# Optimization experiments

Hardware: AMD Instinct MI355X
Metric: run time of the kernel (lower is better)

## Reference

```python
import jax, jax.numpy as jnp
import numpy as np

N, E = 8192, 256
NUM_CLASSES = 4
MARGIN = 0.5
EPS = 1e-8  # torch F.cosine_similarity eps


def setup_inputs() -> dict:
    key = jax.random.key(0)
    k1, k2 = jax.random.split(key)
    inp = jax.random.normal(k1, (N, E), dtype=jnp.float32)
    target = jax.random.randint(k2, (N,), 0, NUM_CLASSES, dtype=jnp.int64)
    return {"input": inp, "target": target}


def reference(input, target):
    n, e = input.shape
    # cosine similarity via normalized matmul (QK^T style) instead of O(N^2 E) broadcast
    norm = jnp.maximum(jnp.linalg.norm(input, axis=1), EPS)
    xn = input / norm[:, None]                      # [N, E]
    cossim = xn @ xn.T                              # [N, N]

    triu = jnp.triu(jnp.ones((n, n), dtype=bool), k=1)  # strict upper triangle

    # initial same_class_mask from binary target; overwritten in the loop below
    binary = target > 0
    same_class_mask = binary[:, None] == binary[None, :]

    same_class_loss = jnp.zeros((), dtype=input.dtype)
    for i in range(NUM_CLASSES):
        is_i = target == i
        cnt = jnp.sum(is_i).astype(input.dtype)
        mask_i = is_i[:, None] == is_i[None, :]     # matches (target==i) vs (target==i) outer equality
        # torch computes target_a == target_b with both being (target==i):
        # equal when both True OR both False
        term = jnp.sum((1.0 - cossim) * (mask_i & triu).astype(input.dtype))
        same_class_loss = same_class_loss + jnp.where(
            cnt > 0, term / jnp.maximum(cnt, 1.0), 0.0
        )
        # torch's loop leaves same_class_mask equal to the last class with counts > 0
        same_class_mask = jnp.where(cnt > 0, mask_i, same_class_mask)

    diff = jax.nn.relu(cossim * (~same_class_mask).astype(input.dtype) - MARGIN)
    diff_class_loss = jnp.sum(diff * triu.astype(input.dtype))

    return (same_class_loss + diff_class_loss) / n
```

## Files before the change

### kernel.cpp

```cpp
#include <hip/hip_runtime.h>

#define NROWS 8192
#define CNT_OFF   0
#define CTR_OFF   16
#define P2_OFF    64
#define H_OFF     4096
#define IDXNL_OFF 8192
#define IDXL_OFF  24576
#define CS_OFF    65536
#define XN_OFF    1048576

typedef __bf16 bf16x8 __attribute__((ext_vector_type(8)));
typedef float  f32x4  __attribute__((ext_vector_type(4)));

__device__ __forceinline__ unsigned short f2bf(float f) {
  unsigned int u = __float_as_uint(f);
  u += 0x7fffu + ((u >> 16) & 1u);
  return (unsigned short)(u >> 16);
}

__device__ __forceinline__ void gl_lds16(const void* g, void* l) {
  __builtin_amdgcn_global_load_lds(
      (const __attribute__((address_space(1))) unsigned int*)g,
      (__attribute__((address_space(3))) unsigned int*)l, 16, 0, 0);
}

__global__ __launch_bounds__(1024) void k_normcs(const float* __restrict__ x,
                                                 const int* __restrict__ tgt,
                                                 unsigned short* __restrict__ xn,
                                                 int* __restrict__ h,
                                                 float* __restrict__ cs) {
  __shared__ float lx[64][256];
  __shared__ int lt[64];
  __shared__ int lh[4];
  const int tid = threadIdx.x, w = tid >> 6, lane = tid & 63;
  const int b = blockIdx.x;
  if (tid < 4) lh[tid] = 0;
  if (tid < 64) lt[tid] = tgt[b * 64 + tid];
#pragma unroll
  for (int i = 0; i < 4; ++i) {
    int r = w * 4 + i;
    int row = b * 64 + r;
    float4 v = reinterpret_cast<const float4*>(x)[row * 64 + lane];
    float ss = v.x * v.x + v.y * v.y + v.z * v.z + v.w * v.w;
#pragma unroll
    for (int off = 32; off; off >>= 1) ss += __shfl_xor(ss, off);
    float iv = 1.0f / fmaxf(sqrtf(ss), 1e-8f);
    float4 nv = make_float4(v.x * iv, v.y * iv, v.z * iv, v.w * iv);
    ushort4 o;
    o.x = f2bf(nv.x); o.y = f2bf(nv.y); o.z = f2bf(nv.z); o.w = f2bf(nv.w);
    reinterpret_cast<ushort4*>(xn)[row * 64 + lane] = o;
    *reinterpret_cast<float4*>(&lx[r][lane * 4]) = nv;
  }
  __syncthreads();
  if (tid < 64) atomicAdd(&lh[lt[tid]], 1);
  {
    const int c = tid >> 8, col = tid & 255;
    float m = 0.0f;
#pragma unroll 8
    for (int r = 0; r < 64; ++r)
      m += (lt[r] == c) ? lx[r][col] : 0.0f;
    cs[b * 1024 + tid] = m;
  }
  __syncthreads();
  if (tid < 4) h[b * 4 + tid] = lh[tid];
}

__global__ __launch_bounds__(256) void k_part(const int* __restrict__ tgt,
                                              const int* __restrict__ h,
                                              int* __restrict__ cnt,
                                              int* __restrict__ ctr,
                                              unsigned short* __restrict__ idxNL,
                                              unsigned short* __restrict__ idxL) {
  __shared__ int lcnt[4], lnb, lwc[4];
  const int tid = threadIdx.x, w = tid >> 6, lane = tid & 63;
  if (tid < 4) lcnt[tid] = 0;
  if (tid == 0) lnb = 0;
  __syncthreads();
  if (tid < 128) {
    int4 hv = ((const int4*)h)[tid];
    atomicAdd(&lcnt[0], hv.x); atomicAdd(&lcnt[1], hv.y);
    atomicAdd(&lcnt[2], hv.z); atomicAdd(&lcnt[3], hv.w);
  }
  __syncthreads();
  int L = 0;
#pragma unroll
  for (int i = 0; i < 4; ++i) if (lcnt[i] > 0) L = i;
  if (tid < 4 * blockIdx.x) atomicAdd(&lnb, h[tid * 4 + L]);
  int r = blockIdx.x * 256 + tid;
  bool isL = (tgt[r] == L);
  unsigned long long mk = __ballot(isL);
  int nl = __popcll(mk);
  if (lane == 0) lwc[w] = nl;
  __syncthreads();
  int baseL = lnb, baseN = blockIdx.x * 256 - lnb;
  for (int w2 = 0; w2 < w; ++w2) { baseL += lwc[w2]; baseN += 64 - lwc[w2]; }
  int pos = __popcll(mk & ((1ull << lane) - 1ull));
  if (isL) idxL[baseL + pos] = (unsigned short)r;
  else     idxNL[baseN + (lane - pos)] = (unsigned short)r;
  if (blockIdx.x == 0 && tid < 4) cnt[tid] = lcnt[tid];
  if (blockIdx.x == 0 && tid == 0) { ctr[1] = lcnt[L]; ctr[0] = NROWS - lcnt[L]; }
}

__global__ __launch_bounds__(256, 2) void k_main(const char* __restrict__ xnb,
                                                 const unsigned short* __restrict__ idxNL,
                                                 const unsigned short* __restrict__ idxL,
                                                 const int* __restrict__ ctr,
                                                 float* __restrict__ partial) {
  __shared__ char lds[2][32768];
  __shared__ float wred[4];

  const int tid = threadIdx.x;
  const int w = tid >> 6, l = tid & 63;
  const int M = ctr[0], NL = ctr[1];
  const int ni = (M + 127) >> 7, nj = (NL + 127) >> 7;
  const int ntiles = ni * nj;

  const int rloc = (l >> 3);
  const unsigned pe = ((unsigned)((l & 7) ^ rloc)) << 4;
  const int wr = (w >> 1) * 64, wc = (w & 1) * 64;
  const int l15 = l & 15;
  const unsigned q16 = ((unsigned)(l >> 4)) << 4;
  const unsigned key = ((unsigned)(l & 7)) << 4;
  const int rowj = (l >> 4) * 4;

  float bsum = 0.0f;
  for (int t = blockIdx.x; t < ntiles; t += gridDim.x) {
    int bi = t / nj, bj = t - bi * nj;
    int rm = min(128, M - bi * 128);
    int rn = min(128, NL - bj * 128);
    bool full = (rm == 128) && (rn == 128);

    unsigned aoff[4], boff[4];
#pragma unroll
    for (int j = 0; j < 4; ++j) {
      int row = (j * 4 + w) * 8 + rloc;
      int ga = idxNL[bi * 128 + min(row, rm - 1)];
      int gb = idxL [bj * 128 + min(row, rn - 1)];
      aoff[j] = (unsigned)ga * 512u + pe;
      boff[j] = (unsigned)gb * 512u + pe;
    }

    auto stage = [&](int buf, int ch) {
      unsigned cbo = (unsigned)(ch << 7);
#pragma unroll
      for (int j = 0; j < 4; ++j)
        gl_lds16(xnb + (size_t)(aoff[j] + cbo), &lds[buf][(j * 4 + w) * 1024]);
#pragma unroll
      for (int j = 0; j < 4; ++j)
        gl_lds16(xnb + (size_t)(boff[j] + cbo), &lds[buf][16384 + (j * 4 + w) * 1024]);
    };

    f32x4 acc[4][4];
#pragma unroll
    for (int m = 0; m < 4; ++m)
#pragma unroll
      for (int n = 0; n < 4; ++n)
        acc[m][n] = (f32x4){0.f, 0.f, 0.f, 0.f};

    auto compute = [&](int buf) {
      const char* bA = lds[buf];
      const char* bB = lds[buf] + 16384;
#pragma unroll
      for (int ks = 0; ks < 2; ++ks) {
        const unsigned q = (unsigned)(ks * 64) + q16;
        bf16x8 af[4], bfr[4];
#pragma unroll
        for (int m = 0; m < 4; ++m)
          af[m] = *(const bf16x8*)(bA + (wr + m * 16 + l15) * 128 + (q ^ key));
#pragma unroll
        for (int n = 0; n < 4; ++n)
          bfr[n] = *(const bf16x8*)(bB + (wc + n * 16 + l15) * 128 + (q ^ key));
        __builtin_amdgcn_s_setprio(1);
#pragma unroll
        for (int m = 0; m < 4; ++m)
#pragma unroll
          for (int n = 0; n < 4; ++n)
            acc[m][n] = __builtin_amdgcn_mfma_f32_16x16x32_bf16(af[m], bfr[n], acc[m][n], 0, 0, 0);
        __builtin_amdgcn_s_setprio(0);
      }
    };

    __syncthreads();
    stage(0, 0); stage(1, 1);
    asm volatile("s_waitcnt vmcnt(8)" ::: "memory");
    __builtin_amdgcn_s_barrier();
    compute(0);
    __builtin_amdgcn_s_barrier();
    stage(0, 2);
    asm volatile("s_waitcnt vmcnt(8)" ::: "memory");
    __builtin_amdgcn_s_barrier();
    compute(1);
    __builtin_amdgcn_s_barrier();
    stage(1, 3);
    asm volatile("s_waitcnt vmcnt(8)" ::: "memory");
    __builtin_amdgcn_s_barrier();
    compute(0);
    __builtin_amdgcn_s_barrier();
    asm volatile("s_waitcnt vmcnt(0)" ::: "memory");
    __builtin_amdgcn_s_barrier();
    compute(1);

    if (full) {
#pragma unroll
      for (int m = 0; m < 4; ++m)
#pragma unroll
        for (int n = 0; n < 4; ++n)
#pragma unroll
          for (int j = 0; j < 4; ++j)
            bsum += fmaxf(acc[m][n][j] - 0.5f, 0.0f);
    } else {
#pragma unroll
      for (int m = 0; m < 4; ++m) {
#pragma unroll
        for (int j = 0; j < 4; ++j) {
          bool rv = (wr + m * 16 + rowj + j) < rm;
#pragma unroll
          for (int n = 0; n < 4; ++n) {
            bool cv = (wc + n * 16 + l15) < rn;
            float g = fmaxf(acc[m][n][j] - 0.5f, 0.0f);
            bsum += (rv && cv) ? g : 0.0f;
          }
        }
      }
    }
  }

#pragma unroll
  for (int off = 32; off; off >>= 1) bsum += __shfl_xor(bsum, off);
  if (l == 0) wred[w] = bsum;
  __syncthreads();
  if (tid == 0)
    partial[blockIdx.x] = wred[0] + wred[1] + wred[2] + wred[3];
}

__global__ __launch_bounds__(256) void k_final(const float* __restrict__ cs,
                                               const int* __restrict__ cnt,
                                               const float* __restrict__ partial2,
                                               float* __restrict__ out) {
  __shared__ float sred[4];
  __shared__ float acc8[8];
  const int tid = threadIdx.x, wv = tid >> 6, lane = tid & 63;

  float m0 = 0, m1 = 0, m2 = 0, m3 = 0;
  for (int b = 0; b < 128; ++b) {
    const float* p = cs + b * 1024;
    m0 += p[tid]; m1 += p[256 + tid]; m2 += p[512 + tid]; m3 += p[768 + tid];
  }
  float T = m0 + m1 + m2 + m3;
  float vals[8];
  vals[0] = m0 * m0; vals[1] = m1 * m1; vals[2] = m2 * m2; vals[3] = m3 * m3;
  vals[4] = (T - m0) * (T - m0); vals[5] = (T - m1) * (T - m1);
  vals[6] = (T - m2) * (T - m2); vals[7] = (T - m3) * (T - m3);
#pragma unroll
  for (int v = 0; v < 8; ++v) {
    float s = vals[v];
#pragma unroll
    for (int off = 32; off; off >>= 1) s += __shfl_xor(s, off);
    if (lane == 0) sred[wv] = s;
    __syncthreads();
    if (tid == 0) acc8[v] = sred[0] + sred[1] + sred[2] + sred[3];
    __syncthreads();
  }
  float s = partial2[tid] + partial2[tid + 256];
#pragma unroll
  for (int off = 32; off; off >>= 1) s += __shfl_xor(s, off);
  if (lane == 0) sred[wv] = s;
  __syncthreads();
  if (tid == 0) {
    double dsum = (double)sred[0] + sred[1] + sred[2] + sred[3];
    double D = (double)NROWS;
    double same = 0.0;
#pragma unroll
    for (int i = 0; i < 4; ++i) {
      int k = cnt[i];
      if (k > 0) {
        double Pi = 0.5 * (double)k * (double)(k - 1)
                  + 0.5 * (double)(NROWS - k) * (double)(NROWS - k - 1);
        double Si = 0.5 * ((double)acc8[i] + (double)acc8[4 + i] - D);
        same += (Pi - Si) / (double)k;
      }
    }
    out[0] = (float)((same + dsum) / (double)NROWS);
  }
}

extern "C" void kernel_launch(void* const* d_in, const int* in_sizes, int n_in,
                              void* d_out, int out_size, void* d_ws, size_t ws_size,
                              hipStream_t stream) {
  (void)in_sizes; (void)n_in; (void)out_size; (void)ws_size;
  const float* x  = (const float*)d_in[0];
  const int* tgt  = (const int*)d_in[1];
  float* out      = (float*)d_out;
  char* ws        = (char*)d_ws;

  int* cnt        = (int*)(ws + CNT_OFF);
  int* ctr        = (int*)(ws + CTR_OFF);
  float* partial2 = (float*)(ws + P2_OFF);
  int* h          = (int*)(ws + H_OFF);
  unsigned short* idxNL = (unsigned short*)(ws + IDXNL_OFF);
  unsigned short* idxL  = (unsigned short*)(ws + IDXL_OFF);
  float* cs       = (float*)(ws + CS_OFF);
  unsigned short* xn = (unsigned short*)(ws + XN_OFF);

  k_normcs<<<128, 1024, 0, stream>>>(x, tgt, xn, h, cs);
  k_part<<<32, 256, 0, stream>>>(tgt, h, cnt, ctr, idxNL, idxL);
  k_main<<<512, 256, 0, stream>>>((const char*)xn, idxNL, idxL, ctr, partial2);
  k_final<<<1, 256, 0, stream>>>(cs, cnt, partial2, out);
}
```

Baseline: 54.01 us.

## Fuse four kernels into one cooperative kernel with grid syncs

Replaces the four separate launches (normalize/class-sums, partition, main GEMM-reduce, final) with one cooperative kernel of 256 blocks that uses grid.sync between phases. The goal is to remove launch gaps and small serial kernels, and to parallelize the class-sum reduction across blocks instead of doing it in a single-block final kernel. In exchange the main GEMM phase runs with 256 blocks instead of 512 and needs a 64KB shared buffer. Grid-wide barriers add their own latency, and cooperative launch limits occupancy.

```diff
diff --git a/kernel.cpp b/kernel.cpp
--- a/kernel.cpp
+++ b/kernel.cpp
@@ -1,14 +1,17 @@
 #include <hip/hip_runtime.h>
+#include <hip/hip_cooperative_groups.h>
+
+namespace cg = cooperative_groups;
 
 #define NROWS 8192
-#define CNT_OFF   0
-#define CTR_OFF   16
-#define P2_OFF    64
-#define H_OFF     4096
+#define NBLK  256
+#define H_OFF     0
 #define IDXNL_OFF 8192
 #define IDXL_OFF  24576
+#define P2_OFF    40960
+#define CSUM_OFF  45056
 #define CS_OFF    65536
-#define XN_OFF    1048576
+#define XN_OFF    2162688
 
 typedef __bf16 bf16x8 __attribute__((ext_vector_type(8)));
 typedef float  f32x4  __attribute__((ext_vector_type(4)));
@@ -25,263 +28,296 @@
       (__attribute__((address_space(3))) unsigned int*)l, 16, 0, 0);
 }
 
-__global__ __launch_bounds__(1024) void k_normcs(const float* __restrict__ x,
-                                                 const int* __restrict__ tgt,
-                                                 unsigned short* __restrict__ xn,
-                                                 int* __restrict__ h,
-                                                 float* __restrict__ cs) {
-  __shared__ float lx[64][256];
-  __shared__ int lt[64];
+__global__ __launch_bounds__(256, 2) void k_all(const float* __restrict__ x,
+                                                const int* __restrict__ tgt,
+                                                char* __restrict__ ws,
+                                                float* __restrict__ out) {
+  __shared__ __align__(16) char sm[65536];
+  __shared__ int lt[32];
   __shared__ int lh[4];
+  __shared__ int scnt[4];
+  __shared__ int spf;
+  __shared__ float wred[8];
+  __shared__ float acc8[8];
+  __shared__ float dsum_s;
+
+  int* h                = (int*)(ws + H_OFF);
+  unsigned short* idxNL = (unsigned short*)(ws + IDXNL_OFF);
+  unsigned short* idxL  = (unsigned short*)(ws + IDXL_OFF);
+  float* partial        = (float*)(ws + P2_OFF);
+  float* csum           = (float*)(ws + CSUM_OFF);
+  float* cs             = (float*)(ws + CS_OFF);
+  unsigned short* xn    = (unsigned short*)(ws + XN_OFF);
+  const char* xnb       = (const char*)xn;
+
+  const int b = blockIdx.x;
   const int tid = threadIdx.x, w = tid >> 6, lane = tid & 63;
-  const int b = blockIdx.x;
-  if (tid < 4) lh[tid] = 0;
-  if (tid < 64) lt[tid] = tgt[b * 64 + tid];
-#pragma unroll
-  for (int i = 0; i < 4; ++i) {
-    int r = w * 4 + i;
-    int row = b * 64 + r;
-    float4 v = reinterpret_cast<const float4*>(x)[row * 64 + lane];
-    float ss = v.x * v.x + v.y * v.y + v.z * v.z + v.w * v.w;
-#pragma unroll
-    for (int off = 32; off; off >>= 1) ss += __shfl_xor(ss, off);
-    float iv = 1.0f / fmaxf(sqrtf(ss), 1e-8f);
-    float4 nv = make_float4(v.x * iv, v.y * iv, v.z * iv, v.w * iv);
-    ushort4 o;
-    o.x = f2bf(nv.x); o.y = f2bf(nv.y); o.z = f2bf(nv.z); o.w = f2bf(nv.w);
-    reinterpret_cast<ushort4*>(xn)[row * 64 + lane] = o;
-    *reinterpret_cast<float4*>(&lx[r][lane * 4]) = nv;
+  cg::grid_group grid = cg::this_grid();
+
+  {
+    float* lx = (float*)sm;
+    if (tid < 32) lt[tid] = tgt[b * 32 + tid];
+    if (tid < 4) lh[tid] = 0;
+#pragma unroll
+    for (int i = 0; i < 8; ++i) {
+      int r = w * 8 + i;
+      int row = b * 32 + r;
+      float4 v = reinterpret_cast<const float4*>(x)[row * 64 + lane];
+      float ss = v.x * v.x + v.y * v.y + v.z * v.z + v.w * v.w;
+#pragma unroll
+      for (int off = 32; off; off >>= 1) ss += __shfl_xor(ss, off);
+      float iv = 1.0f / fmaxf(sqrtf(ss), 1e-8f);
+      float4 nv = make_float4(v.x * iv, v.y * iv, v.z * iv, v.w * iv);
+      ushort4 o;
+      o.x = f2bf(nv.x); o.y = f2bf(nv.y); o.z = f2bf(nv.z); o.w = f2bf(nv.w);
+      reinterpret_cast<ushort4*>(xn)[row * 64 + lane] = o;
+      *reinterpret_cast<float4*>(&lx[r * 256 + lane * 4]) = nv;
+    }
+    __syncthreads();
+    if (tid < 32) atomicAdd(&lh[lt[tid]], 1);
+    {
+      float m0 = 0, m1 = 0, m2 = 0, m3 = 0;
+#pragma unroll
+      for (int r = 0; r < 32; ++r) {
+        float v = lx[r * 256 + tid];
+        int c = lt[r];
+        m0 += (c == 0) ? v : 0.0f;
+        m1 += (c == 1) ? v : 0.0f;
+        m2 += (c == 2) ? v : 0.0f;
+        m3 += (c == 3) ? v : 0.0f;
+      }
+      cs[b * 1024 + tid] = m0;
+      cs[b * 1024 + 256 + tid] = m1;
+      cs[b * 1024 + 512 + tid] = m2;
+      cs[b * 1024 + 768 + tid] = m3;
+    }
+    __syncthreads();
+    if (tid < 4) h[b * 4 + tid] = lh[tid];
   }
-  __syncthreads();
-  if (tid < 64) atomicAdd(&lh[lt[tid]], 1);
+
+  grid.sync();
+
+  int L = 0, M = 0, NLc = 0;
   {
-    const int c = tid >> 8, col = tid & 255;
-    float m = 0.0f;
-#pragma unroll 8
-    for (int r = 0; r < 64; ++r)
-      m += (lt[r] == c) ? lx[r][col] : 0.0f;
-    cs[b * 1024 + tid] = m;
+    if (tid == 0) spf = 0;
+    if (tid < 4) scnt[tid] = 0;
+    __syncthreads();
+    int c0 = 0, c1 = 0, c2 = 0, c3 = 0;
+    const int4* h4 = (const int4*)h;
+    for (int i = tid; i < NBLK; i += 256) {
+      int4 hv = h4[i];
+      c0 += hv.x; c1 += hv.y; c2 += hv.z; c3 += hv.w;
+    }
+#pragma unroll
+    for (int off = 32; off; off >>= 1) {
+      c0 += __shfl_xor(c0, off); c1 += __shfl_xor(c1, off);
+      c2 += __shfl_xor(c2, off); c3 += __shfl_xor(c3, off);
+    }
+    if (lane == 0) {
+      atomicAdd(&scnt[0], c0); atomicAdd(&scnt[1], c1);
+      atomicAdd(&scnt[2], c2); atomicAdd(&scnt[3], c3);
+    }
+    __syncthreads();
+#pragma unroll
+    for (int i = 0; i < 4; ++i) if (scnt[i] > 0) L = i;
+    NLc = scnt[L];
+    M = NROWS - NLc;
+    int pf = 0;
+    for (int i = tid; i < b; i += 256) pf += h[i * 4 + L];
+#pragma unroll
+    for (int off = 32; off; off >>= 1) pf += __shfl_xor(pf, off);
+    if (lane == 0) atomicAdd(&spf, pf);
+    __syncthreads();
+    int baseL = spf, baseN = b * 32 - spf;
+    bool isL = (tid < 32) ? (lt[tid] == L) : false;
+    unsigned long long mk = __ballot((tid < 32) && isL);
+    if (tid < 32) {
+      int pos = __popcll(mk & ((1ull << tid) - 1ull));
+      int row = b * 32 + tid;
+      if (isL) idxL[baseL + pos] = (unsigned short)row;
+      else     idxNL[baseN + (tid - pos)] = (unsigned short)row;
+    }
+#pragma unroll
+    for (int vv = 0; vv < 4; ++vv) {
+      int v = 4 * b + vv;
+      float s = 0.0f;
+      for (int i = tid; i < NBLK; i += 256) s += cs[i * 1024 + v];
+#pragma unroll
+      for (int off = 32; off; off >>= 1) s += __shfl_xor(s, off);
+      if (lane == 0) wred[w] = s;
+      __syncthreads();
+      if (tid == 0) csum[v] = wred[0] + wred[1] + wred[2] + wred[3];
+      __syncthreads();
+    }
   }
-  __syncthreads();
-  if (tid < 4) h[b * 4 + tid] = lh[tid];
-}
-
-__global__ __launch_bounds__(256) void k_part(const int* __restrict__ tgt,
-                                              const int* __restrict__ h,
-                                              int* __restrict__ cnt,
-                                              int* __restrict__ ctr,
-                                              unsigned short* __restrict__ idxNL,
-                                              unsigned short* __restrict__ idxL) {
-  __shared__ int lcnt[4], lnb, lwc[4];
-  const int tid = threadIdx.x, w = tid >> 6, lane = tid & 63;
-  if (tid < 4) lcnt[tid] = 0;
-  if (tid == 0) lnb = 0;
-  __syncthreads();
-  if (tid < 128) {
-    int4 hv = ((const int4*)h)[tid];
-    atomicAdd(&lcnt[0], hv.x); atomicAdd(&lcnt[1], hv.y);
-    atomicAdd(&lcnt[2], hv.z); atomicAdd(&lcnt[3], hv.w);
-  }
-  __syncthreads();
-  int L = 0;
-#pragma unroll
-  for (int i = 0; i < 4; ++i) if (lcnt[i] > 0) L = i;
-  if (tid < 4 * blockIdx.x) atomicAdd(&lnb, h[tid * 4 + L]);
-  int r = blockIdx.x * 256 + tid;
-  bool isL = (tgt[r] == L);
-  unsigned long long mk = __ballot(isL);
-  int nl = __popcll(mk);
-  if (lane == 0) lwc[w] = nl;
-  __syncthreads();
-  int baseL = lnb, baseN = blockIdx.x * 256 - lnb;
-  for (int w2 = 0; w2 < w; ++w2) { baseL += lwc[w2]; baseN += 64 - lwc[w2]; }
-  int pos = __popcll(mk & ((1ull << lane) - 1ull));
-  if (isL) idxL[baseL + pos] = (unsigned short)r;
-  else     idxNL[baseN + (lane - pos)] = (unsigned short)r;
-  if (blockIdx.x == 0 && tid < 4) cnt[tid] = lcnt[tid];
-  if (blockIdx.x == 0 && tid == 0) { ctr[1] = lcnt[L]; ctr[0] = NROWS - lcnt[L]; }
-}
-
-__global__ __launch_bounds__(256, 2) void k_main(const char* __restrict__ xnb,
-                                                 const unsigned short* __restrict__ idxNL,
-                                                 const unsigned short* __restrict__ idxL,
-                                                 const int* __restrict__ ctr,
-                                                 float* __restrict__ partial) {
-  __shared__ char lds[2][32768];
-  __shared__ float wred[4];
-
-  const int tid = threadIdx.x;
-  const int w = tid >> 6, l = tid & 63;
-  const int M = ctr[0], NL = ctr[1];
-  const int ni = (M + 127) >> 7, nj = (NL + 127) >> 7;
-  const int ntiles = ni * nj;
-
-  const int rloc = (l >> 3);
-  const unsigned pe = ((unsigned)((l & 7) ^ rloc)) << 4;
-  const int wr = (w >> 1) * 64, wc = (w & 1) * 64;
-  const int l15 = l & 15;
-  const unsigned q16 = ((unsigned)(l >> 4)) << 4;
-  const unsigned key = ((unsigned)(l & 7)) << 4;
-  const int rowj = (l >> 4) * 4;
-
-  float bsum = 0.0f;
-  for (int t = blockIdx.x; t < ntiles; t += gridDim.x) {
-    int bi = t / nj, bj = t - bi * nj;
-    int rm = min(128, M - bi * 128);
-    int rn = min(128, NL - bj * 128);
-    bool full = (rm == 128) && (rn == 128);
-
-    unsigned aoff[4], boff[4];
-#pragma unroll
-    for (int j = 0; j < 4; ++j) {
-      int row = (j * 4 + w) * 8 + rloc;
-      int ga = idxNL[bi * 128 + min(row, rm - 1)];
-      int gb = idxL [bj * 128 + min(row, rn - 1)];
-      aoff[j] = (unsigned)ga * 512u + pe;
-      boff[j] = (unsigned)gb * 512u + pe;
-    }
-
-    auto stage = [&](int buf, int ch) {
-      unsigned cbo = (unsigned)(ch << 7);
-#pragma unroll
-      for (int j = 0; j < 4; ++j)
-        gl_lds16(xnb + (size_t)(aoff[j] + cbo), &lds[buf][(j * 4 + w) * 1024]);
-#pragma unroll
-      for (int j = 0; j < 4; ++j)
-        gl_lds16(xnb + (size_t)(boff[j] + cbo), &lds[buf][16384 + (j * 4 + w) * 1024]);
-    };
-
-    f32x4 acc[4][4];
-#pragma unroll
-    for (int m = 0; m < 4; ++m)
-#pragma unroll
-      for (int n = 0; n < 4; ++n)
-        acc[m][n] = (f32x4){0.f, 0.f, 0.f, 0.f};
-
-    auto compute = [&](int buf) {
-      const char* bA = lds[buf];
-      const char* bB = lds[buf] + 16384;
-#pragma unroll
-      for (int ks = 0; ks < 2; ++ks) {
-        const unsigned q = (unsigned)(ks * 64) + q16;
-        bf16x8 af[4], bfr[4];
+
+  grid.sync();
+
+  {
+    char (*lds)[32768] = (char(*)[32768])sm;
+    const int ni = (M + 127) >> 7, nj = (NLc + 127) >> 7;
+    const int ntiles = ni * nj;
+
+    const int rl = lane >> 3;
+    const unsigned pe = ((unsigned)((lane & 7) ^ rl)) << 4;
+    const int wr = (w >> 1) * 64, wc = (w & 1) * 64;
+    const int l15 = lane & 15;
+    const unsigned q16 = ((unsigned)(lane >> 4)) << 4;
+    const unsigned key = ((unsigned)(lane & 7)) << 4;
+    const int rowj = (lane >> 4) * 4;
+
+    float bsum = 0.0f;
+    for (int t = b; t < ntiles; t += NBLK) {
+      int bi = t / nj, bj = t - bi * nj;
+      int rm = min(128, M - bi * 128);
+      int rn = min(128, NLc - bj * 128);
+      bool full = (rm == 128) && (rn == 128);
+
+      unsigned aoff[4], boff[4];
+#pragma unroll
+      for (int j = 0; j < 4; ++j) {
+        int row = (j * 4 + w) * 8 + rl;
+        int ga = idxNL[bi * 128 + min(row, rm - 1)];
+        int gb = idxL [bj * 128 + min(row, rn - 1)];
+        aoff[j] = (unsigned)ga * 512u + pe;
+        boff[j] = (unsigned)gb * 512u + pe;
+      }
+
+      auto stage = [&](int buf, int ch) {
+        unsigned cbo = (unsigned)(ch << 7);
+#pragma unroll
+        for (int j = 0; j < 4; ++j)
+          gl_lds16(xnb + (size_t)(aoff[j] + cbo), &lds[buf][(j * 4 + w) * 1024]);
+#pragma unroll
+        for (int j = 0; j < 4; ++j)
+          gl_lds16(xnb + (size_t)(boff[j] + cbo), &lds[buf][16384 + (j * 4 + w) * 1024]);
+      };
+
+      f32x4 acc[4][4];
+#pragma unroll
+      for (int m = 0; m < 4; ++m)
+#pragma unroll
+        for (int n = 0; n < 4; ++n)
+          acc[m][n] = (f32x4){0.f, 0.f, 0.f, 0.f};
+
+      auto compute = [&](int buf) {
+        const char* bA = lds[buf];
+        const char* bB = lds[buf] + 16384;
+#pragma unroll
+        for (int ks = 0; ks < 2; ++ks) {
+          const unsigned q = (unsigned)(ks * 64) + q16;
+          bf16x8 af[4], bfr[4];
+#pragma unroll
+          for (int m = 0; m < 4; ++m)
+            af[m] = *(const bf16x8*)(bA + (wr + m * 16 + l15) * 128 + (q ^ key));
+#pragma unroll
+          for (int n = 0; n < 4; ++n)
+            bfr[n] = *(const bf16x8*)(bB + (wc + n * 16 + l15) * 128 + (q ^ key));
+          __builtin_amdgcn_s_setprio(1);
+#pragma unroll
+          for (int m = 0; m < 4; ++m)
+#pragma unroll
+            for (int n = 0; n < 4; ++n)
+              acc[m][n] = __builtin_amdgcn_mfma_f32_16x16x32_bf16(af[m], bfr[n], acc[m][n], 0, 0, 0);
+          __builtin_amdgcn_s_setprio(0);
+        }
+      };
+
+      __syncthreads();
+      stage(0, 0); stage(1, 1);
+      asm volatile("s_waitcnt vmcnt(8)" ::: "memory");
+      __builtin_amdgcn_s_barrier();
+      compute(0);
+      __builtin_amdgcn_s_barrier();
+      stage(0, 2);
+      asm volatile("s_waitcnt vmcnt(8)" ::: "memory");
+      __builtin_amdgcn_s_barrier();
+      compute(1);
+      __builtin_amdgcn_s_barrier();
+      stage(1, 3);
+      asm volatile("s_waitcnt vmcnt(8)" ::: "memory");
+      __builtin_amdgcn_s_barrier();
+      compute(0);
+      __builtin_amdgcn_s_barrier();
+      asm volatile("s_waitcnt vmcnt(0)" ::: "memory");
+      __builtin_amdgcn_s_barrier();
+      compute(1);
+
+      if (full) {
 #pragma unroll
         for (int m = 0; m < 4; ++m)
-          af[m] = *(const bf16x8*)(bA + (wr + m * 16 + l15) * 128 + (q ^ key));
-#pragma unroll
-        for (int n = 0; n < 4; ++n)
-          bfr[n] = *(const bf16x8*)(bB + (wc + n * 16 + l15) * 128 + (q ^ key));
-        __builtin_amdgcn_s_setprio(1);
-#pragma unroll
-        for (int m = 0; m < 4; ++m)
 #pragma unroll
           for (int n = 0; n < 4; ++n)
-            acc[m][n] = __builtin_amdgcn_mfma_f32_16x16x32_bf16(af[m], bfr[n], acc[m][n], 0, 0, 0);
-        __builtin_amdgcn_s_setprio(0);
-      }
-    };
-
-    __syncthreads();
-    stage(0, 0); stage(1, 1);
-    asm volatile("s_waitcnt vmcnt(8)" ::: "memory");
-    __builtin_amdgcn_s_barrier();
-    compute(0);
-    __builtin_amdgcn_s_barrier();
-    stage(0, 2);
-    asm volatile("s_waitcnt vmcnt(8)" ::: "memory");
-    __builtin_amdgcn_s_barrier();
-    compute(1);
-    __builtin_amdgcn_s_barrier();
-    stage(1, 3);
-    asm volatile("s_waitcnt vmcnt(8)" ::: "memory");
-    __builtin_amdgcn_s_barrier();
-    compute(0);
-    __builtin_amdgcn_s_barrier();
-    asm volatile("s_waitcnt vmcnt(0)" ::: "memory");
-    __builtin_amdgcn_s_barrier();
-    compute(1);
-
-    if (full) {
-#pragma unroll
-      for (int m = 0; m < 4; ++m)
-#pragma unroll
-        for (int n = 0; n < 4; ++n)
-#pragma unroll
-          for (int j = 0; j < 4; ++j)
-            bsum += fmaxf(acc[m][n][j] - 0.5f, 0.0f);
-    } else {
-#pragma unroll
-      for (int m = 0; m < 4; ++m) {
-#pragma unroll
-        for (int j = 0; j < 4; ++j) {
-          bool rv = (wr + m * 16 + rowj + j) < rm;
-#pragma unroll
-          for (int n = 0; n < 4; ++n) {
-            bool cv = (wc + n * 16 + l15) < rn;
-            float g = fmaxf(acc[m][n][j] - 0.5f, 0.0f);
-            bsum += (rv && cv) ? g : 0.0f;
+#pragma unroll
+            for (int j = 0; j < 4; ++j)
+              bsum += fmaxf(acc[m][n][j] - 0.5f, 0.0f);
+      } else {
+#pragma unroll
+        for (int m = 0; m < 4; ++m) {
+#pragma unroll
+          for (int j = 0; j < 4; ++j) {
+            bool rv = (wr + m * 16 + rowj + j) < rm;
+#pragma unroll
+            for (int n = 0; n < 4; ++n) {
+              bool cv = (wc + n * 16 + l15) < rn;
+              float g = fmaxf(acc[m][n][j] - 0.5f, 0.0f);
+              bsum += (rv && cv) ? g : 0.0f;
+            }
           }
         }
       }
     }
+
+#pragma unroll
+    for (int off = 32; off; off >>= 1) bsum += __shfl_xor(bsum, off);
+    if (lane == 0) wred[w] = bsum;
+    __syncthreads();
+    if (tid == 0) partial[b] = wred[0] + wred[1] + wred[2] + wred[3];
   }
 
-#pragma unroll
-  for (int off = 32; off; off >>= 1) bsum += __shfl_xor(bsum, off);
-  if (l == 0) wred[w] = bsum;
-  __syncthreads();
-  if (tid == 0)
-    partial[blockIdx.x] = wred[0] + wred[1] + wred[2] + wred[3];
-}
-
-__global__ __launch_bounds__(256) void k_final(const float* __restrict__ cs,
-                                               const int* __restrict__ cnt,
-                                               const float* __restrict__ partial2,
-                                               float* __restrict__ out) {
-  __shared__ float sred[4];
-  __shared__ float acc8[8];
-  const int tid = threadIdx.x, wv = tid >> 6, lane = tid & 63;
-
-  float m0 = 0, m1 = 0, m2 = 0, m3 = 0;
-  for (int b = 0; b < 128; ++b) {
-    const float* p = cs + b * 1024;
-    m0 += p[tid]; m1 += p[256 + tid]; m2 += p[512 + tid]; m3 += p[768 + tid];
-  }
-  float T = m0 + m1 + m2 + m3;
-  float vals[8];
-  vals[0] = m0 * m0; vals[1] = m1 * m1; vals[2] = m2 * m2; vals[3] = m3 * m3;
-  vals[4] = (T - m0) * (T - m0); vals[5] = (T - m1) * (T - m1);
-  vals[6] = (T - m2) * (T - m2); vals[7] = (T - m3) * (T - m3);
-#pragma unroll
-  for (int v = 0; v < 8; ++v) {
-    float s = vals[v];
+  grid.sync();
+
+  if (b == 0) {
+    float s = partial[tid];
 #pragma unroll
     for (int off = 32; off; off >>= 1) s += __shfl_xor(s, off);
-    if (lane == 0) sred[wv] = s;
-    __syncthreads();
-    if (tid == 0) acc8[v] = sred[0] + sred[1] + sred[2] + sred[3];
-    __syncthreads();
-  }
-  float s = partial2[tid] + partial2[tid + 256];
-#pragma unroll
-  for (int off = 32; off; off >>= 1) s += __shfl_xor(s, off);
-  if (lane == 0) sred[wv] = s;
-  __syncthreads();
-  if (tid == 0) {
-    double dsum = (double)sred[0] + sred[1] + sred[2] + sred[3];
-    double D = (double)NROWS;
-    double same = 0.0;
-#pragma unroll
-    for (int i = 0; i < 4; ++i) {
-      int k = cnt[i];
-      if (k > 0) {
-        double Pi = 0.5 * (double)k * (double)(k - 1)
-                  + 0.5 * (double)(NROWS - k) * (double)(NROWS - k - 1);
-        double Si = 0.5 * ((double)acc8[i] + (double)acc8[4 + i] - D);
-        same += (Pi - Si) / (double)k;
+    if (lane == 0) wred[w] = s;
+    __syncthreads();
+    if (tid == 0) dsum_s = wred[0] + wred[1] + wred[2] + wred[3];
+    __syncthreads();
+
+    float m0 = csum[tid], m1 = csum[256 + tid], m2 = csum[512 + tid], m3 = csum[768 + tid];
+    float T = m0 + m1 + m2 + m3;
+    float vals[8];
+    vals[0] = m0 * m0; vals[1] = m1 * m1; vals[2] = m2 * m2; vals[3] = m3 * m3;
+    vals[4] = (T - m0) * (T - m0); vals[5] = (T - m1) * (T - m1);
+    vals[6] = (T - m2) * (T - m2); vals[7] = (T - m3) * (T - m3);
+#pragma unroll
+    for (int v = 0; v < 8; ++v) {
+      float sv = vals[v];
+#pragma unroll
+      for (int off = 32; off; off >>= 1) sv += __shfl_xor(sv, off);
+      if (lane == 0) wred[w] = sv;
+      __syncthreads();
+      if (tid == 0) acc8[v] = wred[0] + wred[1] + wred[2] + wred[3];
+      __syncthreads();
+    }
+    if (tid == 0) {
+      double dsum = (double)dsum_s;
+      double D = (double)NROWS;
+      double same = 0.0;
+#pragma unroll
+      for (int i = 0; i < 4; ++i) {
+        int k = scnt[i];
+        if (k > 0) {
+          double Pi = 0.5 * (double)k * (double)(k - 1)
+                    + 0.5 * (double)(NROWS - k) * (double)(NROWS - k - 1);
+          double Si = 0.5 * ((double)acc8[i] + (double)acc8[4 + i] - D);
+          same += (Pi - Si) / (double)k;
+        }
       }
-    }
-    out[0] = (float)((same + dsum) / (double)NROWS);
+      out[0] = (float)((same + dsum) / (double)NROWS);
+    }
   }
 }
 
@@ -294,17 +330,7 @@
   float* out      = (float*)d_out;
   char* ws        = (char*)d_ws;
 
-  int* cnt        = (int*)(ws + CNT_OFF);
-  int* ctr        = (int*)(ws + CTR_OFF);
-  float* partial2 = (float*)(ws + P2_OFF);
-  int* h          = (int*)(ws + H_OFF);
-  unsigned short* idxNL = (unsigned short*)(ws + IDXNL_OFF);
-  unsigned short* idxL  = (unsigned short*)(ws + IDXL_OFF);
-  float* cs       = (float*)(ws + CS_OFF);
-  unsigned short* xn = (unsigned short*)(ws + XN_OFF);
-
-  k_normcs<<<128, 1024, 0, stream>>>(x, tgt, xn, h, cs);
-  k_part<<<32, 256, 0, stream>>>(tgt, h, cnt, ctr, idxNL, idxL);
-  k_main<<<512, 256, 0, stream>>>((const char*)xn, idxNL, idxL, ctr, partial2);
-  k_final<<<1, 256, 0, stream>>>(cs, cnt, partial2, out);
+  void* args[] = { (void*)&x, (void*)&tgt, (void*)&ws, (void*)&out };
+  (void)hipLaunchCooperativeKernel(reinterpret_cast<const void*>(&k_all),
+                                   dim3(NBLK), dim3(256), args, 0, stream);
 }
```

Result: slower. 131.5 us (+143.5%).
